# Kernel optimization log

Measured on AMD Instinct MI355X. Metric: run time of the kernel, lower is better.

## Reference

```python
import jax, jax.numpy as jnp
import numpy as np

B = 16384
D = 1024          # entity_dim
N_LAYERS = 4
TEMPERATURE = 32.0  # sqrt(entity_dim)


def setup_inputs() -> dict:
    key = jax.random.key(0)
    ks = jax.random.split(key, 6)
    d2 = 2 * D
    scale = 1.0 / np.sqrt(d2)
    x1 = jax.random.normal(ks[0], (B, D), dtype=jnp.float32)
    x2 = jax.random.normal(ks[1], (B, D), dtype=jnp.float32)
    # stacked per-layer Linear(2D, 2D) params; torch Linear stores W as [out, in]
    Ws = jax.random.normal(ks[2], (N_LAYERS, d2, d2), dtype=jnp.float32) * scale
    bs = jax.random.normal(ks[3], (N_LAYERS, d2), dtype=jnp.float32) * scale
    W_last = jax.random.normal(ks[4], (D, d2), dtype=jnp.float32) * scale
    b_last = jax.random.normal(ks[5], (D,), dtype=jnp.float32) * scale
    return {"x1": x1, "x2": x2, "Ws": Ws, "bs": bs, "W_last": W_last, "b_last": b_last}


def reference(x1, x2, Ws, bs, W_last, b_last):
    # x: [B, 2, D]
    x = jnp.stack((x1, x2), axis=1)
    # attn: [B, 2, 2] -- tiny self-attention over the 2 tokens
    attn = jnp.einsum('bsd,btd->bst', x / TEMPERATURE, x)
    attn = jax.nn.softmax(attn, axis=-1)  # dropout = identity in eval mode
    x = jnp.einsum('bst,btd->bsd', attn, x)
    # concat the two attended tokens -> [B, 2D]
    h = jnp.concatenate((x[:, 0, :], x[:, 1, :]), axis=-1)
    for i in range(N_LAYERS):
        h = jax.nn.relu(h @ Ws[i].T + bs[i])
    return h @ W_last.T + b_last
```

## Files before the change

### kernel.cpp

```cpp
#include <hip/hip_runtime.h>

typedef __bf16 bf16x8 __attribute__((ext_vector_type(8)));
typedef float f32x4 __attribute__((ext_vector_type(4)));

__device__ __forceinline__ unsigned short f2bf(float f) {
    unsigned int u = __builtin_bit_cast(unsigned int, f);
    u += 0x7FFFu + ((u >> 16) & 1u);
    return (unsigned short)(u >> 16);
}

__global__ void cvt_kernel(const float* __restrict__ in,
                           unsigned short* __restrict__ out, long n4) {
    long i = (long)blockIdx.x * blockDim.x + threadIdx.x;
    long stride = (long)gridDim.x * blockDim.x;
    for (; i < n4; i += stride) {
        float4 v = ((const float4*)in)[i];
        ushort4 o;
        o.x = f2bf(v.x); o.y = f2bf(v.y); o.z = f2bf(v.z); o.w = f2bf(v.w);
        ((ushort4*)out)[i] = o;
    }
}

__global__ __launch_bounds__(256) void attn_kernel(
    const float* __restrict__ x1, const float* __restrict__ x2,
    unsigned short* __restrict__ h) {
    const int D = 1024;
    const int lane = threadIdx.x & 63;
    const int wave = threadIdx.x >> 6;
    const long row = (long)blockIdx.x * 4 + wave;
    const float4* p1 = (const float4*)(x1 + row * D);
    const float4* p2 = (const float4*)(x2 + row * D);
    float4 v1[4], v2[4];
    float s11 = 0.f, s12 = 0.f, s22 = 0.f;
#pragma unroll
    for (int j = 0; j < 4; ++j) {
        v1[j] = p1[lane + 64 * j];
        v2[j] = p2[lane + 64 * j];
        s11 += v1[j].x * v1[j].x + v1[j].y * v1[j].y + v1[j].z * v1[j].z + v1[j].w * v1[j].w;
        s12 += v1[j].x * v2[j].x + v1[j].y * v2[j].y + v1[j].z * v2[j].z + v1[j].w * v2[j].w;
        s22 += v2[j].x * v2[j].x + v2[j].y * v2[j].y + v2[j].z * v2[j].z + v2[j].w * v2[j].w;
    }
#pragma unroll
    for (int off = 1; off < 64; off <<= 1) {
        s11 += __shfl_xor(s11, off);
        s12 += __shfl_xor(s12, off);
        s22 += __shfl_xor(s22, off);
    }
    const float a00 = 1.f / (1.f + expf((s12 - s11) * (1.f / 32.f)));
    const float a10 = 1.f / (1.f + expf((s22 - s12) * (1.f / 32.f)));
    const float a01 = 1.f - a00, a11 = 1.f - a10;
    unsigned short* h0 = h + row * 2048;
#pragma unroll
    for (int j = 0; j < 4; ++j) {
        const int f = lane + 64 * j;
        ushort4 o0, o1;
        o0.x = f2bf(a00 * v1[j].x + a01 * v2[j].x);
        o0.y = f2bf(a00 * v1[j].y + a01 * v2[j].y);
        o0.z = f2bf(a00 * v1[j].z + a01 * v2[j].z);
        o0.w = f2bf(a00 * v1[j].w + a01 * v2[j].w);
        o1.x = f2bf(a10 * v1[j].x + a11 * v2[j].x);
        o1.y = f2bf(a10 * v1[j].y + a11 * v2[j].y);
        o1.z = f2bf(a10 * v1[j].z + a11 * v2[j].z);
        o1.w = f2bf(a10 * v1[j].w + a11 * v2[j].w);
        ((ushort4*)(h0))[f] = o0;
        ((ushort4*)(h0 + 1024))[f] = o1;
    }
}

#define BAR   __builtin_amdgcn_s_barrier()
#define LGKM0 asm volatile("s_waitcnt lgkmcnt(0)" ::: "memory")
#define VMW6  asm volatile("s_waitcnt vmcnt(6)" ::: "memory")
#define VMW0  asm volatile("s_waitcnt vmcnt(0)" ::: "memory")
#define PRIO1 __builtin_amdgcn_s_setprio(1)
#define PRIO0 __builtin_amdgcn_s_setprio(0)

#define MMQ(mb)                                                                \
  _Pragma("unroll") for (int n = 0; n < 4; ++n)                                \
  _Pragma("unroll") for (int mq = 0; mq < 4; ++mq)                             \
    acc[(mb) + mq][n] = __builtin_amdgcn_mfma_f32_16x16x32_bf16(               \
        Bf[n], Af[mq], acc[(mb) + mq][n], 0, 0, 0);

template <bool RELU, typename OT>
__global__ __launch_bounds__(512, 2) void gemm256(
    const unsigned short* __restrict__ A,
    const unsigned short* __restrict__ Bw,
    const float* __restrict__ bias,
    OT* __restrict__ C,
    int N, int K) {
    __shared__ __align__(16) unsigned short lds[65536];
    const int tid = threadIdx.x;
    const int lane = tid & 63, wave = tid >> 6;
    const int wm = wave >> 2, wn = wave & 3;
    const int fr = lane & 15, fq = lane >> 4;

    const int cpx = (int)gridDim.x >> 3;
    const int swz = ((int)blockIdx.x & 7) * cpx + ((int)blockIdx.x >> 3);
    const int bm = swz & 63;
    const int bn = swz >> 6;
    const long m0 = (long)bm * 256, n0 = (long)bn * 256;
    const long rowb = (long)K * 2;

    const int flip = ((fr >> 3) & 1) << 5;
    const int lbase = fr * 64 + ((fq * 16) ^ flip);
    const int aRd = wm * 8192 + lbase;
    const int bRd = 32768 + wn * 4096 + lbase;
    const char* ldsc = (const char*)lds;

    const int srow = wave * 16 + (lane >> 2);
    const int scol = ((lane & 3) << 4) ^ ((lane >> 5) << 5);
    const char* Abl = (const char*)A + m0 * rowb;
    const char* Bbl = (const char*)Bw + n0 * rowb;

    auto stage = [&](const char* mb, int regbase, int kh, int kt) {
#pragma unroll
        for (int L = 0; L < 2; ++L) {
            const int r = L * 128 + srow;
            const char* src = mb + (long)r * rowb + kt * 128 + kh * 64 + scol;
            __builtin_amdgcn_global_load_lds(
                (const __attribute__((address_space(1))) void*)src,
                (__attribute__((address_space(3))) void*)((char*)lds +
                    (regbase + kh * 16384 + L * 8192 + wave * 1024)),
                16, 0, 0);
        }
    };

    f32x4 acc[8][4] = {};
    bf16x8 Bf[4], Af[4];

    auto rdB = [&](int Tb, int kh) {
        const int b = Tb + kh * 16384 + bRd;
#pragma unroll
        for (int nf = 0; nf < 4; ++nf)
            Bf[nf] = *(const bf16x8*)(ldsc + b + nf * 1024);
    };
    auto rdA = [&](int Tb, int kh, int mh) {
        const int b = Tb + kh * 16384 + aRd + mh * 4096;
#pragma unroll
        for (int mq = 0; mq < 4; ++mq)
            Af[mq] = *(const bf16x8*)(ldsc + b + mq * 1024);
    };

    stage(Bbl, 32768, 0, 0); stage(Abl, 0, 0, 0);
    stage(Bbl, 32768, 1, 0); stage(Abl, 0, 1, 0);
    stage(Bbl, 65536 + 32768, 0, 1); stage(Abl, 65536, 0, 1);
    stage(Bbl, 65536 + 32768, 1, 1);
    VMW6;
    BAR;

    const int NT = K >> 6, NIT = NT >> 1;
    for (int i = 0; i < NIT; ++i) {
        const int u = 2 * i + 1, t2 = 2 * i + 2, t3 = 2 * i + 3;
        const bool g = (i + 1 < NIT);

        rdB(0, 0); rdA(0, 0, 0);
        stage(Abl, 65536, 1, u);
        BAR; LGKM0; PRIO1; MMQ(0); PRIO0; BAR;

        rdA(0, 0, 1);
        if (g) stage(Bbl, 32768, 0, t2);
        BAR; LGKM0; PRIO1; MMQ(4); PRIO0; BAR;

        rdB(0, 1); rdA(0, 1, 0);
        if (g) stage(Abl, 0, 0, t2);
        BAR; LGKM0; PRIO1; MMQ(0); PRIO0; BAR;

        rdA(0, 1, 1);
        if (g) stage(Bbl, 32768, 1, t2);
        BAR; LGKM0; PRIO1; MMQ(4); PRIO0;
        if (g) { VMW6; } else { VMW0; }
        BAR;

        rdB(65536, 0); rdA(65536, 0, 0);
        if (g) stage(Abl, 0, 1, t2);
        BAR; LGKM0; PRIO1; MMQ(0); PRIO0; BAR;

        rdA(65536, 0, 1);
        if (g) stage(Bbl, 65536 + 32768, 0, t3);
        BAR; LGKM0; PRIO1; MMQ(4); PRIO0; BAR;

        rdB(65536, 1); rdA(65536, 1, 0);
        if (g) stage(Abl, 65536, 0, t3);
        BAR; LGKM0; PRIO1; MMQ(0); PRIO0; BAR;

        rdA(65536, 1, 1);
        if (g) stage(Bbl, 65536 + 32768, 1, t3);
        BAR; LGKM0; PRIO1; MMQ(4); PRIO0;
        if (g) { VMW6; } else { VMW0; }
        BAR;
    }

    const long crow0 = m0 + wm * 128 + fr;
    const long ccol0 = n0 + wn * 64 + fq * 4;
    float4 bv[4];
#pragma unroll
    for (int n = 0; n < 4; ++n) bv[n] = *(const float4*)(bias + ccol0 + n * 16);
#pragma unroll
    for (int m = 0; m < 8; ++m) {
        const long rb = (crow0 + m * 16) * N;
#pragma unroll
        for (int n = 0; n < 4; ++n) {
            float v0 = acc[m][n][0] + bv[n].x;
            float v1 = acc[m][n][1] + bv[n].y;
            float v2 = acc[m][n][2] + bv[n].z;
            float v3 = acc[m][n][3] + bv[n].w;
            if (RELU) {
                v0 = v0 > 0.f ? v0 : 0.f; v1 = v1 > 0.f ? v1 : 0.f;
                v2 = v2 > 0.f ? v2 : 0.f; v3 = v3 > 0.f ? v3 : 0.f;
            }
            if constexpr (sizeof(OT) == 2) {
                uint2 oo;
                oo.x = (unsigned)f2bf(v0) | ((unsigned)f2bf(v1) << 16);
                oo.y = (unsigned)f2bf(v2) | ((unsigned)f2bf(v3) << 16);
                *(uint2*)((unsigned short*)C + rb + ccol0 + n * 16) = oo;
            } else {
                *(float4*)((float*)C + rb + ccol0 + n * 16) =
                    make_float4(v0, v1, v2, v3);
            }
        }
    }
}

extern "C" void kernel_launch(void* const* d_in, const int* in_sizes, int n_in,
                              void* d_out, int out_size, void* d_ws, size_t ws_size,
                              hipStream_t stream) {
    const float* x1 = (const float*)d_in[0];
    const float* x2 = (const float*)d_in[1];
    const float* Ws = (const float*)d_in[2];
    const float* bs = (const float*)d_in[3];
    const float* Wl = (const float*)d_in[4];
    const float* bl = (const float*)d_in[5];
    float* out = (float*)d_out;

    char* ws = (char*)d_ws;
    unsigned short* hA  = (unsigned short*)(ws);
    unsigned short* hB  = (unsigned short*)(ws + (67108864L));
    unsigned short* Wbf = (unsigned short*)(ws + (134217728L));
    unsigned short* Wlb = (unsigned short*)(ws + (167772160L));

    cvt_kernel<<<2048, 256, 0, stream>>>(Ws, Wbf, 4L * 2048 * 2048 / 4);
    cvt_kernel<<<512, 256, 0, stream>>>(Wl, Wlb, 1024L * 2048 / 4);

    attn_kernel<<<16384 / 4, 256, 0, stream>>>(x1, x2, hA);

    gemm256<true, unsigned short><<<512, 512, 0, stream>>>(hA, Wbf + 0L * 2048 * 2048, bs + 0 * 2048, hB, 2048, 2048);
    gemm256<true, unsigned short><<<512, 512, 0, stream>>>(hB, Wbf + 1L * 2048 * 2048, bs + 1 * 2048, hA, 2048, 2048);
    gemm256<true, unsigned short><<<512, 512, 0, stream>>>(hA, Wbf + 2L * 2048 * 2048, bs + 2 * 2048, hB, 2048, 2048);
    gemm256<true, unsigned short><<<512, 512, 0, stream>>>(hB, Wbf + 3L * 2048 * 2048, bs + 3 * 2048, hA, 2048, 2048);
    gemm256<false, float><<<256, 512, 0, stream>>>(hA, Wlb, bl, out, 1024, 2048);
}
```

Baseline: 672.4 us.

## Double-buffer LDS fragment registers and use partial waitcnts in GEMM main loop

The GEMM loop now keeps two sets of A/B fragment registers. Each phase issues the LDS reads for the next MFMA block before computing the current one, and waits only with partial lgkmcnt counts, so LDS read latency overlaps MFMA work. Global-to-LDS vmcnt waits are spread across every phase instead of every fourth, and the first fragments are prefetched before the loop. This raises register pressure and makes correctness depend on hand-tuned wait counts.

```diff
diff --git a/kernel.cpp b/kernel.cpp
--- a/kernel.cpp
+++ b/kernel.cpp
@@ -68,17 +68,17 @@
 }
 
 #define BAR   __builtin_amdgcn_s_barrier()
-#define LGKM0 asm volatile("s_waitcnt lgkmcnt(0)" ::: "memory")
-#define VMW6  asm volatile("s_waitcnt vmcnt(6)" ::: "memory")
-#define VMW0  asm volatile("s_waitcnt vmcnt(0)" ::: "memory")
+#define SB0   __builtin_amdgcn_sched_barrier(0)
+#define LGKM(n) do { asm volatile("s_waitcnt lgkmcnt(" #n ")" ::: "memory"); SB0; } while (0)
+#define VMW(n)  asm volatile("s_waitcnt vmcnt(" #n ")" ::: "memory")
 #define PRIO1 __builtin_amdgcn_s_setprio(1)
 #define PRIO0 __builtin_amdgcn_s_setprio(0)
 
-#define MMQ(mb)                                                                \
+#define MMQ(mb, BS, AS)                                                        \
   _Pragma("unroll") for (int n = 0; n < 4; ++n)                                \
   _Pragma("unroll") for (int mq = 0; mq < 4; ++mq)                             \
     acc[(mb) + mq][n] = __builtin_amdgcn_mfma_f32_16x16x32_bf16(               \
-        Bf[n], Af[mq], acc[(mb) + mq][n], 0, 0, 0);
+        BS[n], AS[mq], acc[(mb) + mq][n], 0, 0, 0);
 
 template <bool RELU, typename OT>
 __global__ __launch_bounds__(512, 2) void gemm256(
@@ -125,67 +125,85 @@
     };
 
     f32x4 acc[8][4] = {};
-    bf16x8 Bf[4], Af[4];
-
-    auto rdB = [&](int Tb, int kh) {
+    bf16x8 Bs0[4], Bs1[4], As0[4], As1[4];
+
+    auto rdB = [&](int Tb, int kh, bf16x8 (&D)[4]) {
         const int b = Tb + kh * 16384 + bRd;
 #pragma unroll
         for (int nf = 0; nf < 4; ++nf)
-            Bf[nf] = *(const bf16x8*)(ldsc + b + nf * 1024);
+            D[nf] = *(const bf16x8*)(ldsc + b + nf * 1024);
     };
-    auto rdA = [&](int Tb, int kh, int mh) {
+    auto rdA = [&](int Tb, int kh, int mh, bf16x8 (&D)[4]) {
         const int b = Tb + kh * 16384 + aRd + mh * 4096;
 #pragma unroll
         for (int mq = 0; mq < 4; ++mq)
-            Af[mq] = *(const bf16x8*)(ldsc + b + mq * 1024);
+            D[mq] = *(const bf16x8*)(ldsc + b + mq * 1024);
     };
 
-    stage(Bbl, 32768, 0, 0); stage(Abl, 0, 0, 0);
-    stage(Bbl, 32768, 1, 0); stage(Abl, 0, 1, 0);
-    stage(Bbl, 65536 + 32768, 0, 1); stage(Abl, 65536, 0, 1);
+    stage(Bbl, 32768, 0, 0);
+    stage(Abl, 0, 0, 0);
+    stage(Bbl, 32768, 1, 0);
+    stage(Abl, 0, 1, 0);
+    stage(Bbl, 65536 + 32768, 0, 1);
+    stage(Abl, 65536, 0, 1);
     stage(Bbl, 65536 + 32768, 1, 1);
-    VMW6;
+    VMW(10);
     BAR;
+    rdB(0, 0, Bs0); rdA(0, 0, 0, As0);
 
     const int NT = K >> 6, NIT = NT >> 1;
     for (int i = 0; i < NIT; ++i) {
         const int u = 2 * i + 1, t2 = 2 * i + 2, t3 = 2 * i + 3;
         const bool g = (i + 1 < NIT);
 
-        rdB(0, 0); rdA(0, 0, 0);
+        rdA(0, 0, 1, As1);
         stage(Abl, 65536, 1, u);
-        BAR; LGKM0; PRIO1; MMQ(0); PRIO0; BAR;
-
-        rdA(0, 0, 1);
+        BAR; LGKM(4); PRIO1; MMQ(0, Bs0, As0); PRIO0; VMW(6); BAR;
+
+        rdB(0, 1, Bs1); rdA(0, 1, 0, As0);
         if (g) stage(Bbl, 32768, 0, t2);
-        BAR; LGKM0; PRIO1; MMQ(4); PRIO0; BAR;
-
-        rdB(0, 1); rdA(0, 1, 0);
+        BAR; LGKM(8); PRIO1; MMQ(4, Bs0, As1); PRIO0;
+        if (g) { VMW(6); } else { VMW(4); }
+        BAR;
+
+        rdA(0, 1, 1, As1);
         if (g) stage(Abl, 0, 0, t2);
-        BAR; LGKM0; PRIO1; MMQ(0); PRIO0; BAR;
-
-        rdA(0, 1, 1);
+        BAR; LGKM(4); PRIO1; MMQ(0, Bs1, As0); PRIO0;
+        if (g) { VMW(6); } else { VMW(2); }
+        BAR;
+
+        rdB(65536, 0, Bs0); rdA(65536, 0, 0, As0);
         if (g) stage(Bbl, 32768, 1, t2);
-        BAR; LGKM0; PRIO1; MMQ(4); PRIO0;
-        if (g) { VMW6; } else { VMW0; }
-        BAR;
-
-        rdB(65536, 0); rdA(65536, 0, 0);
+        BAR; LGKM(8); PRIO1; MMQ(4, Bs1, As1); PRIO0;
+        if (g) { VMW(6); } else { VMW(0); }
+        BAR;
+
+        rdA(65536, 0, 1, As1);
         if (g) stage(Abl, 0, 1, t2);
-        BAR; LGKM0; PRIO1; MMQ(0); PRIO0; BAR;
-
-        rdA(65536, 0, 1);
+        BAR; LGKM(4); PRIO1; MMQ(0, Bs0, As0); PRIO0;
+        if (g) VMW(6);
+        BAR;
+
+        rdB(65536, 1, Bs1); rdA(65536, 1, 0, As0);
         if (g) stage(Bbl, 65536 + 32768, 0, t3);
-        BAR; LGKM0; PRIO1; MMQ(4); PRIO0; BAR;
-
-        rdB(65536, 1); rdA(65536, 1, 0);
+        BAR; LGKM(8); PRIO1; MMQ(4, Bs0, As1); PRIO0;
+        if (g) VMW(6);
+        BAR;
+
+        rdA(65536, 1, 1, As1);
         if (g) stage(Abl, 65536, 0, t3);
-        BAR; LGKM0; PRIO1; MMQ(0); PRIO0; BAR;
-
-        rdA(65536, 1, 1);
-        if (g) stage(Bbl, 65536 + 32768, 1, t3);
-        BAR; LGKM0; PRIO1; MMQ(4); PRIO0;
-        if (g) { VMW6; } else { VMW0; }
+        BAR; LGKM(4); PRIO1; MMQ(0, Bs1, As0); PRIO0;
+        if (g) VMW(6);
+        BAR;
+
+        if (g) {
+            rdB(0, 0, Bs0); rdA(0, 0, 0, As0);
+            stage(Bbl, 65536 + 32768, 1, t3);
+        }
+        BAR;
+        if (g) { LGKM(8); } else { LGKM(0); }
+        PRIO1; MMQ(4, Bs1, As1); PRIO0;
+        if (g) VMW(6);
         BAR;
     }
 
```

Result: slower. 686.0 us (+2.0%).

## Replace 256x256 GEMM tile with 128x256 tile and triple-buffered single-barrier loop

Applied to the files above, without the earlier changes.

Shrinks the GEMM block tile from 256x256 to 128x256 with a 32-wide K step, and cuts LDS to 72KB so up to four blocks fit per CU. The phased double-buffer schedule with many barriers becomes a simple triple-buffered pipeline with one barrier per K step. This aims to raise occupancy and wave count while removing barrier overhead. The cost is lower arithmetic intensity per block, so each block does more global loading per FLOP.

```diff
diff --git a/kernel.cpp b/kernel.cpp
--- a/kernel.cpp
+++ b/kernel.cpp
@@ -68,26 +68,19 @@
 }
 
 #define BAR   __builtin_amdgcn_s_barrier()
-#define LGKM0 asm volatile("s_waitcnt lgkmcnt(0)" ::: "memory")
-#define VMW6  asm volatile("s_waitcnt vmcnt(6)" ::: "memory")
+#define VMW3  asm volatile("s_waitcnt vmcnt(3)" ::: "memory")
 #define VMW0  asm volatile("s_waitcnt vmcnt(0)" ::: "memory")
 #define PRIO1 __builtin_amdgcn_s_setprio(1)
 #define PRIO0 __builtin_amdgcn_s_setprio(0)
 
-#define MMQ(mb)                                                                \
-  _Pragma("unroll") for (int n = 0; n < 4; ++n)                                \
-  _Pragma("unroll") for (int mq = 0; mq < 4; ++mq)                             \
-    acc[(mb) + mq][n] = __builtin_amdgcn_mfma_f32_16x16x32_bf16(               \
-        Bf[n], Af[mq], acc[(mb) + mq][n], 0, 0, 0);
-
 template <bool RELU, typename OT>
-__global__ __launch_bounds__(512, 2) void gemm256(
+__global__ __launch_bounds__(512, 4) void gemm128(
     const unsigned short* __restrict__ A,
     const unsigned short* __restrict__ Bw,
     const float* __restrict__ bias,
     OT* __restrict__ C,
     int N, int K) {
-    __shared__ __align__(16) unsigned short lds[65536];
+    __shared__ __align__(16) unsigned short lds[36864];
     const int tid = threadIdx.x;
     const int lane = tid & 63, wave = tid >> 6;
     const int wm = wave >> 2, wn = wave & 3;
@@ -95,114 +88,87 @@
 
     const int cpx = (int)gridDim.x >> 3;
     const int swz = ((int)blockIdx.x & 7) * cpx + ((int)blockIdx.x >> 3);
-    const int bm = swz & 63;
-    const int bn = swz >> 6;
-    const long m0 = (long)bm * 256, n0 = (long)bn * 256;
+    const int bm = swz & 127;
+    const int bn = swz >> 7;
+    const long m0 = (long)bm * 128, n0 = (long)bn * 256;
     const long rowb = (long)K * 2;
 
     const int flip = ((fr >> 3) & 1) << 5;
     const int lbase = fr * 64 + ((fq * 16) ^ flip);
-    const int aRd = wm * 8192 + lbase;
-    const int bRd = 32768 + wn * 4096 + lbase;
+    const int aRd = wm * 4096 + lbase;
+    const int bRd = 8192 + wn * 4096 + lbase;
     const char* ldsc = (const char*)lds;
 
-    const int srow = wave * 16 + (lane >> 2);
+    const int srow = lane >> 2;
     const int scol = ((lane & 3) << 4) ^ ((lane >> 5) << 5);
     const char* Abl = (const char*)A + m0 * rowb;
     const char* Bbl = (const char*)Bw + n0 * rowb;
-
-    auto stage = [&](const char* mb, int regbase, int kh, int kt) {
-#pragma unroll
-        for (int L = 0; L < 2; ++L) {
-            const int r = L * 128 + srow;
-            const char* src = mb + (long)r * rowb + kt * 128 + kh * 64 + scol;
-            __builtin_amdgcn_global_load_lds(
-                (const __attribute__((address_space(1))) void*)src,
-                (__attribute__((address_space(3))) void*)((char*)lds +
-                    (regbase + kh * 16384 + L * 8192 + wave * 1024)),
-                16, 0, 0);
-        }
+    const char* s0 = Abl + (long)(wave * 16 + srow) * rowb + scol;
+    const char* s1 = Bbl + (long)(wave * 16 + srow) * rowb + scol;
+    const char* s2 = Bbl + (long)(128 + wave * 16 + srow) * rowb + scol;
+    const int d0 = wave * 1024 + lane * 16;
+    const int d1 = 8192 + wave * 1024 + lane * 16;
+    const int d2 = 16384 + wave * 1024 + lane * 16;
+
+    auto gl = [&](const char* src, int dst) {
+        __builtin_amdgcn_global_load_lds(
+            (const __attribute__((address_space(1))) void*)src,
+            (__attribute__((address_space(3))) void*)((char*)lds + dst),
+            16, 0, 0);
     };
-
-    f32x4 acc[8][4] = {};
-    bf16x8 Bf[4], Af[4];
-
-    auto rdB = [&](int Tb, int kh) {
-        const int b = Tb + kh * 16384 + bRd;
+    auto stage = [&](int kt, int slot) {
+        const long ko = (long)kt * 64;
+        const int sb = slot * 24576;
+        gl(s0 + ko, sb + d0);
+        gl(s1 + ko, sb + d1);
+        gl(s2 + ko, sb + d2);
+    };
+
+    f32x4 acc[4][4] = {};
+    bf16x8 Af[4], Bf[4];
+
+    stage(0, 0);
+    stage(1, 1);
+    VMW3;
+    BAR;
+
+    const int NT = K >> 5;
+    int sl = 0;
+    for (int t = 0; t < NT; ++t) {
+        const bool g = (t + 2 < NT);
+        if (g) { const int ss = (sl == 0) ? 2 : sl - 1; stage(t + 2, ss); }
+        const int sb = sl * 24576;
+#pragma unroll
+        for (int mq = 0; mq < 4; ++mq)
+            Af[mq] = *(const bf16x8*)(ldsc + sb + aRd + mq * 1024);
 #pragma unroll
         for (int nf = 0; nf < 4; ++nf)
-            Bf[nf] = *(const bf16x8*)(ldsc + b + nf * 1024);
-    };
-    auto rdA = [&](int Tb, int kh, int mh) {
-        const int b = Tb + kh * 16384 + aRd + mh * 4096;
-#pragma unroll
-        for (int mq = 0; mq < 4; ++mq)
-            Af[mq] = *(const bf16x8*)(ldsc + b + mq * 1024);
-    };
-
-    stage(Bbl, 32768, 0, 0); stage(Abl, 0, 0, 0);
-    stage(Bbl, 32768, 1, 0); stage(Abl, 0, 1, 0);
-    stage(Bbl, 65536 + 32768, 0, 1); stage(Abl, 65536, 0, 1);
-    stage(Bbl, 65536 + 32768, 1, 1);
-    VMW6;
-    BAR;
-
-    const int NT = K >> 6, NIT = NT >> 1;
-    for (int i = 0; i < NIT; ++i) {
-        const int u = 2 * i + 1, t2 = 2 * i + 2, t3 = 2 * i + 3;
-        const bool g = (i + 1 < NIT);
-
-        rdB(0, 0); rdA(0, 0, 0);
-        stage(Abl, 65536, 1, u);
-        BAR; LGKM0; PRIO1; MMQ(0); PRIO0; BAR;
-
-        rdA(0, 0, 1);
-        if (g) stage(Bbl, 32768, 0, t2);
-        BAR; LGKM0; PRIO1; MMQ(4); PRIO0; BAR;
-
-        rdB(0, 1); rdA(0, 1, 0);
-        if (g) stage(Abl, 0, 0, t2);
-        BAR; LGKM0; PRIO1; MMQ(0); PRIO0; BAR;
-
-        rdA(0, 1, 1);
-        if (g) stage(Bbl, 32768, 1, t2);
-        BAR; LGKM0; PRIO1; MMQ(4); PRIO0;
-        if (g) { VMW6; } else { VMW0; }
+            Bf[nf] = *(const bf16x8*)(ldsc + sb + bRd + nf * 1024);
+        PRIO1;
+#pragma unroll
+        for (int nf = 0; nf < 4; ++nf)
+#pragma unroll
+            for (int mq = 0; mq < 4; ++mq)
+                acc[mq][nf] = __builtin_amdgcn_mfma_f32_16x16x32_bf16(
+                    Bf[nf], Af[mq], acc[mq][nf], 0, 0, 0);
+        PRIO0;
+        if (g) { VMW3; } else { VMW0; }
         BAR;
-
-        rdB(65536, 0); rdA(65536, 0, 0);
-        if (g) stage(Abl, 0, 1, t2);
-        BAR; LGKM0; PRIO1; MMQ(0); PRIO0; BAR;
-
-        rdA(65536, 0, 1);
-        if (g) stage(Bbl, 65536 + 32768, 0, t3);
-        BAR; LGKM0; PRIO1; MMQ(4); PRIO0; BAR;
-
-        rdB(65536, 1); rdA(65536, 1, 0);
-        if (g) stage(Abl, 65536, 0, t3);
-        BAR; LGKM0; PRIO1; MMQ(0); PRIO0; BAR;
-
-        rdA(65536, 1, 1);
-        if (g) stage(Bbl, 65536 + 32768, 1, t3);
-        BAR; LGKM0; PRIO1; MMQ(4); PRIO0;
-        if (g) { VMW6; } else { VMW0; }
-        BAR;
-    }
-
-    const long crow0 = m0 + wm * 128 + fr;
+        sl = (sl == 2) ? 0 : sl + 1;
+    }
+
+    const long crow0 = m0 + wm * 64 + fr;
     const long ccol0 = n0 + wn * 64 + fq * 4;
-    float4 bv[4];
-#pragma unroll
-    for (int n = 0; n < 4; ++n) bv[n] = *(const float4*)(bias + ccol0 + n * 16);
-#pragma unroll
-    for (int m = 0; m < 8; ++m) {
+#pragma unroll
+    for (int m = 0; m < 4; ++m) {
         const long rb = (crow0 + m * 16) * N;
 #pragma unroll
         for (int n = 0; n < 4; ++n) {
-            float v0 = acc[m][n][0] + bv[n].x;
-            float v1 = acc[m][n][1] + bv[n].y;
-            float v2 = acc[m][n][2] + bv[n].z;
-            float v3 = acc[m][n][3] + bv[n].w;
+            const float4 bv = *(const float4*)(bias + ccol0 + n * 16);
+            float v0 = acc[m][n][0] + bv.x;
+            float v1 = acc[m][n][1] + bv.y;
+            float v2 = acc[m][n][2] + bv.z;
+            float v3 = acc[m][n][3] + bv.w;
             if (RELU) {
                 v0 = v0 > 0.f ? v0 : 0.f; v1 = v1 > 0.f ? v1 : 0.f;
                 v2 = v2 > 0.f ? v2 : 0.f; v3 = v3 > 0.f ? v3 : 0.f;
@@ -242,9 +208,9 @@
 
     attn_kernel<<<16384 / 4, 256, 0, stream>>>(x1, x2, hA);
 
-    gemm256<true, unsigned short><<<512, 512, 0, stream>>>(hA, Wbf + 0L * 2048 * 2048, bs + 0 * 2048, hB, 2048, 2048);
-    gemm256<true, unsigned short><<<512, 512, 0, stream>>>(hB, Wbf + 1L * 2048 * 2048, bs + 1 * 2048, hA, 2048, 2048);
-    gemm256<true, unsigned short><<<512, 512, 0, stream>>>(hA, Wbf + 2L * 2048 * 2048, bs + 2 * 2048, hB, 2048, 2048);
-    gemm256<true, unsigned short><<<512, 512, 0, stream>>>(hB, Wbf + 3L * 2048 * 2048, bs + 3 * 2048, hA, 2048, 2048);
-    gemm256<false, float><<<256, 512, 0, stream>>>(hA, Wlb, bl, out, 1024, 2048);
-}
+    gemm128<true, unsigned short><<<1024, 512, 0, stream>>>(hA, Wbf + 0L * 2048 * 2048, bs + 0 * 2048, hB, 2048, 2048);
+    gemm128<true, unsigned short><<<1024, 512, 0, stream>>>(hB, Wbf + 1L * 2048 * 2048, bs + 1 * 2048, hA, 2048, 2048);
+    gemm128<true, unsigned short><<<1024, 512, 0, stream>>>(hA, Wbf + 2L * 2048 * 2048, bs + 2 * 2048, hB, 2048, 2048);
+    gemm128<true, unsigned short><<<1024, 512, 0, stream>>>(hB, Wbf + 3L * 2048 * 2048, bs + 3 * 2048, hA, 2048, 2048);
+    gemm128<false, float><<<512, 512, 0, stream>>>(hA, Wlb, bl, out, 1024, 2048);
+}
```

Result: slower. 732.3 us (+8.9%).

## Restructure GEMM main loop into single-barrier phases with peeled tail

Applied to the files above, without the earlier changes.

Rewrites the 256x256 bf16 MFMA GEMM main loop so each phase issues one global-to-LDS stage, reads fragments, waits with a fixed vmcnt and then runs a single barrier before the MFMAs. This halves the barriers per phase, removes the per-phase conditional staging by peeling the last iteration, and drops the s_setprio toggles. It also changes the block swizzle so N-tiles vary fastest, with a shift that depends on N, to improve operand reuse in L2. The fixed-count waits and the reordered stage/read sequence risk LDS read/write hazards if the counts are wrong.

```diff
diff --git a/kernel.cpp b/kernel.cpp
--- a/kernel.cpp
+++ b/kernel.cpp
@@ -68,11 +68,9 @@
 }
 
 #define BAR   __builtin_amdgcn_s_barrier()
-#define LGKM0 asm volatile("s_waitcnt lgkmcnt(0)" ::: "memory")
-#define VMW6  asm volatile("s_waitcnt vmcnt(6)" ::: "memory")
-#define VMW0  asm volatile("s_waitcnt vmcnt(0)" ::: "memory")
-#define PRIO1 __builtin_amdgcn_s_setprio(1)
-#define PRIO0 __builtin_amdgcn_s_setprio(0)
+#define LGKM0 do { asm volatile("s_waitcnt lgkmcnt(0)" ::: "memory"); \
+                   __builtin_amdgcn_sched_barrier(0); } while (0)
+#define VMW(n) asm volatile("s_waitcnt vmcnt(" #n ")" ::: "memory")
 
 #define MMQ(mb)                                                                \
   _Pragma("unroll") for (int n = 0; n < 4; ++n)                                \
@@ -93,10 +91,12 @@
     const int wm = wave >> 2, wn = wave & 3;
     const int fr = lane & 15, fq = lane >> 4;
 
+    const int nbn = N >> 8;
+    const int sh = (nbn == 8) ? 3 : 2;
     const int cpx = (int)gridDim.x >> 3;
     const int swz = ((int)blockIdx.x & 7) * cpx + ((int)blockIdx.x >> 3);
-    const int bm = swz & 63;
-    const int bn = swz >> 6;
+    const int bn = swz & (nbn - 1);
+    const int bm = swz >> sh;
     const long m0 = (long)bm * 256, n0 = (long)bn * 256;
     const long rowb = (long)K * 2;
 
@@ -140,53 +140,63 @@
             Af[mq] = *(const bf16x8*)(ldsc + b + mq * 1024);
     };
 
-    stage(Bbl, 32768, 0, 0); stage(Abl, 0, 0, 0);
-    stage(Bbl, 32768, 1, 0); stage(Abl, 0, 1, 0);
-    stage(Bbl, 65536 + 32768, 0, 1); stage(Abl, 65536, 0, 1);
-    stage(Bbl, 65536 + 32768, 1, 1);
-    VMW6;
+    stage(Bbl, 32768, 0, 0);
+    stage(Abl, 0,     0, 0);
+    stage(Bbl, 32768, 1, 0);
+    stage(Abl, 0,     1, 0);
+    stage(Bbl, 65536 + 32768, 0, 1);
+    stage(Abl, 65536,         0, 1);
+    VMW(8);
     BAR;
 
     const int NT = K >> 6, NIT = NT >> 1;
-    for (int i = 0; i < NIT; ++i) {
+    for (int i = 0; i < NIT - 1; ++i) {
         const int u = 2 * i + 1, t2 = 2 * i + 2, t3 = 2 * i + 3;
-        const bool g = (i + 1 < NIT);
-
+        stage(Bbl, 65536 + 32768, 1, u);
         rdB(0, 0); rdA(0, 0, 0);
+        VMW(8); BAR; LGKM0; MMQ(0);
         stage(Abl, 65536, 1, u);
-        BAR; LGKM0; PRIO1; MMQ(0); PRIO0; BAR;
-
         rdA(0, 0, 1);
-        if (g) stage(Bbl, 32768, 0, t2);
-        BAR; LGKM0; PRIO1; MMQ(4); PRIO0; BAR;
-
+        VMW(8); BAR; LGKM0; MMQ(4);
+        stage(Bbl, 32768, 0, t2);
         rdB(0, 1); rdA(0, 1, 0);
-        if (g) stage(Abl, 0, 0, t2);
-        BAR; LGKM0; PRIO1; MMQ(0); PRIO0; BAR;
-
+        VMW(8); BAR; LGKM0; MMQ(0);
+        stage(Abl, 0, 0, t2);
         rdA(0, 1, 1);
-        if (g) stage(Bbl, 32768, 1, t2);
-        BAR; LGKM0; PRIO1; MMQ(4); PRIO0;
-        if (g) { VMW6; } else { VMW0; }
-        BAR;
-
+        VMW(8); BAR; LGKM0; MMQ(4);
+        stage(Bbl, 32768, 1, t2);
         rdB(65536, 0); rdA(65536, 0, 0);
-        if (g) stage(Abl, 0, 1, t2);
-        BAR; LGKM0; PRIO1; MMQ(0); PRIO0; BAR;
-
+        VMW(8); BAR; LGKM0; MMQ(0);
+        stage(Abl, 0, 1, t2);
         rdA(65536, 0, 1);
-        if (g) stage(Bbl, 65536 + 32768, 0, t3);
-        BAR; LGKM0; PRIO1; MMQ(4); PRIO0; BAR;
-
+        VMW(8); BAR; LGKM0; MMQ(4);
+        stage(Bbl, 65536 + 32768, 0, t3);
         rdB(65536, 1); rdA(65536, 1, 0);
-        if (g) stage(Abl, 65536, 0, t3);
-        BAR; LGKM0; PRIO1; MMQ(0); PRIO0; BAR;
-
+        VMW(8); BAR; LGKM0; MMQ(0);
+        stage(Abl, 65536, 0, t3);
         rdA(65536, 1, 1);
-        if (g) stage(Bbl, 65536 + 32768, 1, t3);
-        BAR; LGKM0; PRIO1; MMQ(4); PRIO0;
-        if (g) { VMW6; } else { VMW0; }
-        BAR;
+        VMW(8); BAR; LGKM0; MMQ(4);
+    }
+    {
+        const int u = NT - 1;
+        stage(Bbl, 65536 + 32768, 1, u);
+        rdB(0, 0); rdA(0, 0, 0);
+        VMW(8); BAR; LGKM0; MMQ(0);
+        stage(Abl, 65536, 1, u);
+        rdA(0, 0, 1);
+        VMW(8); BAR; LGKM0; MMQ(4);
+        rdB(0, 1); rdA(0, 1, 0);
+        VMW(8); BAR; LGKM0; MMQ(0);
+        rdA(0, 1, 1);
+        VMW(4); BAR; LGKM0; MMQ(4);
+        rdB(65536, 0); rdA(65536, 0, 0);
+        VMW(4); BAR; LGKM0; MMQ(0);
+        rdA(65536, 0, 1);
+        VMW(0); BAR; LGKM0; MMQ(4);
+        rdB(65536, 1); rdA(65536, 1, 0);
+        VMW(0); BAR; LGKM0; MMQ(0);
+        rdA(65536, 1, 1);
+        VMW(0); BAR; LGKM0; MMQ(4);
     }
 
     const long crow0 = m0 + wm * 128 + fr;
```

Measured after the change: 597.9 us. 1.12x faster.
